# Optimization experiments

Hardware: AMD Instinct MI355X
Metric: run time of the kernel (lower is better)

Reference implementation:

```python
import jax, jax.numpy as jnp
import numpy as np

B, L1, L2, D = 128, 256, 256, 768
NEG = -10000.0
EPS = 1e-8


def setup_inputs() -> dict:
    key = jax.random.key(0)
    k1, k2, k3, k4 = jax.random.split(key, 4)
    v1 = jax.random.normal(k1, (B, L1, D), dtype=jnp.float32)
    v2 = jax.random.normal(k2, (B, L2, D), dtype=jnp.float32)
    # masks from random valid lengths in [L//2, L]
    len1 = jax.random.randint(k3, (B,), L1 // 2, L1 + 1)
    len2 = jax.random.randint(k4, (B,), L2 // 2, L2 + 1)
    mask1 = (jnp.arange(L1)[None, :] < len1[:, None]).astype(jnp.float32)
    mask2 = (jnp.arange(L2)[None, :] < len2[:, None]).astype(jnp.float32)
    return {"v1": v1, "mask1": mask1, "v2": v2, "mask2": mask2}


def reference(v1, mask1, v2, mask2):
    # alignment matrix [B, L1, L2]
    match = jnp.einsum('bld,bmd->blm', v1, v2)
    pair_mask = (mask1[:, :, None] * mask2[:, None, :]) > 0
    match = jnp.where(pair_mask, match, NEG)
    # attention over side 1: negative max-pool over L2, scaled
    s1 = -jnp.max(match, axis=2) / 100.0            # [B, L1]
    s1 = jnp.where(mask1 > 0, s1, NEG)
    attn1 = jax.nn.softmax(s1, axis=1)
    p1 = jnp.einsum('bld,bl->bd', v1, attn1)        # [B, D]
    # attention over side 2: negative max-pool over L1, scaled
    s2 = -jnp.max(match, axis=1) / 100.0            # [B, L2]
    s2 = jnp.where(mask2 > 0, s2, NEG)
    attn2 = jax.nn.softmax(s2, axis=1)
    p2 = jnp.einsum('bmd,bm->bd', v2, attn2)        # [B, D]
    # torch.nn.functional.cosine_similarity semantics (per-vector norm clamp)
    n1 = jnp.maximum(jnp.linalg.norm(p1, axis=-1), EPS)
    n2 = jnp.maximum(jnp.linalg.norm(p2, axis=-1), EPS)
    return jnp.sum(p1 * p2, axis=-1) / (n1 * n2)
```

## Files before the change

### kernel.cpp

```cpp
#include <hip/hip_runtime.h>


#define B_   128
#define L_   256
#define D_   768
#define NEGV (-10000.0f)

typedef _Float16 f16x8 __attribute__((ext_vector_type(8)));
typedef __fp16   h16x2 __attribute__((ext_vector_type(2)));
typedef float    f32x4 __attribute__((ext_vector_type(4)));

#define BT   128
#define BKF  64
#define NKT  (D_ / BKF)
#define LDH  72

__device__ __forceinline__ unsigned fmap(float f) {
    unsigned u = __float_as_uint(f);
    return (u & 0x80000000u) ? ~u : (u | 0x80000000u);
}
__device__ __forceinline__ float fdecode(unsigned u) {
    return __uint_as_float((u & 0x80000000u) ? (u ^ 0x80000000u) : ~u);
}
__device__ __forceinline__ float wred_max(float v) {
    #pragma unroll
    for (int o = 32; o; o >>= 1) v = fmaxf(v, __shfl_xor(v, o));
    return v;
}
__device__ __forceinline__ float wred_sum(float v) {
    #pragma unroll
    for (int o = 32; o; o >>= 1) v += __shfl_xor(v, o);
    return v;
}

__device__ __forceinline__ f16x8 cvt8(float4 a, float4 b) {
    union { h16x2 h2[4]; f16x8 h8; } u;
    u.h2[0] = __builtin_amdgcn_cvt_pkrtz(a.x, a.y);
    u.h2[1] = __builtin_amdgcn_cvt_pkrtz(a.z, a.w);
    u.h2[2] = __builtin_amdgcn_cvt_pkrtz(b.x, b.y);
    u.h2[3] = __builtin_amdgcn_cvt_pkrtz(b.z, b.w);
    return u.h8;
}

__global__ __launch_bounds__(512, 2)
void k_match_max(const float* __restrict__ v1, const float* __restrict__ m1,
                 const float* __restrict__ v2, const float* __restrict__ m2,
                 unsigned* __restrict__ ru1, unsigned* __restrict__ ru2)
{
    __shared__ __align__(16) _Float16 As[2][BT * LDH];
    __shared__ __align__(16) _Float16 Bs[2][BT * LDH];
    __shared__ unsigned rU[BT], cU[BT];
    __shared__ float m1s[BT], m2s[BT];

    const int bid = blockIdx.x;
    const int wg  = (bid & 7) * 64 + (bid >> 3);
    const int b = wg >> 2, ti = (wg >> 1) & 1, tj = wg & 1;

    const int t = threadIdx.x;
    const int lane = t & 63, w = t >> 6;
    const int wr = w >> 1, wc = w & 1;
    const int fr = lane & 15, fg = lane >> 4;

    if (t < BT) {
        rU[t] = 0u; cU[t] = 0u;
        m1s[t] = m1[b * L_ + ti * BT + t];
        m2s[t] = m2[b * L_ + tj * BT + t];
    }

    const int grow = t >> 2;
    const int c4   = t & 3;
    const float* ga = v1 + ((size_t)b * L_ + ti * BT + grow) * D_ + c4 * 16;
    const float* gb = v2 + ((size_t)b * L_ + tj * BT + grow) * D_ + c4 * 16;

    float4 ra[4], rb[4];

    #define GLOAD(kt) do {                                                    \
        const float* A_ = ga + (kt) * BKF;                                    \
        const float* C_ = gb + (kt) * BKF;                                    \
        ra[0] = *(const float4*)(A_);      ra[1] = *(const float4*)(A_ + 4);  \
        ra[2] = *(const float4*)(A_ + 8);  ra[3] = *(const float4*)(A_ + 12); \
        rb[0] = *(const float4*)(C_);      rb[1] = *(const float4*)(C_ + 4);  \
        rb[2] = *(const float4*)(C_ + 8);  rb[3] = *(const float4*)(C_ + 12); \
    } while (0)

    #define DSWRITE(buf) do {                                                 \
        _Float16* da = &As[buf][grow * LDH + c4 * 16];                        \
        _Float16* db = &Bs[buf][grow * LDH + c4 * 16];                        \
        *(f16x8*)da       = cvt8(ra[0], ra[1]);                               \
        *(f16x8*)(da + 8) = cvt8(ra[2], ra[3]);                               \
        *(f16x8*)db       = cvt8(rb[0], rb[1]);                               \
        *(f16x8*)(db + 8) = cvt8(rb[2], rb[3]);                               \
    } while (0)

    f32x4 acc[2][4] = {};
    GLOAD(0);
    DSWRITE(0);
    __syncthreads();
    int cur = 0;
    for (int kt = 0; kt < NKT; ++kt) {
        if (kt + 1 < NKT) GLOAD(kt + 1);
        __builtin_amdgcn_sched_barrier(0);
        #pragma unroll
        for (int ks = 0; ks < 2; ++ks) {
            f16x8 af[2], bf[4];
            #pragma unroll
            for (int i = 0; i < 2; ++i) {
                int r1 = wr * 32 + i * 16 + fr;
                af[i] = *(const f16x8*)&As[cur][r1 * LDH + ks * 32 + fg * 8];
            }
            #pragma unroll
            for (int j = 0; j < 4; ++j) {
                int r2 = wc * 64 + j * 16 + fr;
                bf[j] = *(const f16x8*)&Bs[cur][r2 * LDH + ks * 32 + fg * 8];
            }
            #pragma unroll
            for (int i = 0; i < 2; ++i)
                #pragma unroll
                for (int j = 0; j < 4; ++j)
                    acc[i][j] = __builtin_amdgcn_mfma_f32_16x16x32_f16(af[i], bf[j], acc[i][j], 0, 0, 0);
        }
        __builtin_amdgcn_sched_barrier(0);
        if (kt + 1 < NKT) DSWRITE(cur ^ 1);
        __syncthreads();
        cur ^= 1;
    }
    #undef GLOAD
    #undef DSWRITE

    #pragma unroll
    for (int i = 0; i < 2; ++i)
        #pragma unroll
        for (int r = 0; r < 4; ++r) {
            int row = wr * 32 + i * 16 + fg * 4 + r;
            bool rv = m1s[row] > 0.f;
            float mx = NEGV;
            #pragma unroll
            for (int j = 0; j < 4; ++j) {
                int col = wc * 64 + j * 16 + fr;
                float vv = (rv && m2s[col] > 0.f) ? acc[i][j][r] : NEGV;
                mx = fmaxf(mx, vv);
            }
            atomicMax(&rU[row], fmap(mx));
        }
    #pragma unroll
    for (int j = 0; j < 4; ++j) {
        int col = wc * 64 + j * 16 + fr;
        bool cv = m2s[col] > 0.f;
        float mx = NEGV;
        #pragma unroll
        for (int i = 0; i < 2; ++i)
            #pragma unroll
            for (int r = 0; r < 4; ++r) {
                int row = wr * 32 + i * 16 + fg * 4 + r;
                float vv = (cv && m1s[row] > 0.f) ? acc[i][j][r] : NEGV;
                mx = fmaxf(mx, vv);
            }
        atomicMax(&cU[col], fmap(mx));
    }
    __syncthreads();
    if (t < BT)            atomicMax(&ru1[b * L_ + ti * BT + t], rU[t]);
    else if (t < 2 * BT)   atomicMax(&ru2[b * L_ + tj * BT + (t - BT)], cU[t - BT]);
}

__global__ __launch_bounds__(256)
void k_attn_pool(const float* __restrict__ v1, const float* __restrict__ m1,
                 const float* __restrict__ v2, const float* __restrict__ m2,
                 const unsigned* __restrict__ ru1, const unsigned* __restrict__ ru2,
                 float* __restrict__ pout)
{
    const int lin = (int)blockIdx.x;
    const int swz = (lin & 7) * 96 + (lin >> 3);
    const int b = swz / 6, rem = swz % 6, side = rem / 3, chunk = rem % 3;

    const float* v     = side ? v2 : v1;
    const float* mk    = side ? m2 : m1;
    const unsigned* ru = side ? ru2 : ru1;
    const int t = threadIdx.x, lane = t & 63, w = t >> 6;

    __shared__ float attn[L_];
    __shared__ float sred[4];

    float mkv = mk[b * L_ + t];
    float s = (mkv > 0.f) ? (-fdecode(ru[b * L_ + t]) / 100.0f) : NEGV;

    float wm = wred_max(s);
    if (lane == 0) sred[w] = wm;
    __syncthreads();
    float mx = fmaxf(fmaxf(sred[0], sred[1]), fmaxf(sred[2], sred[3]));
    float e = expf(s - mx);
    __syncthreads();
    float ws = wred_sum(e);
    if (lane == 0) sred[w] = ws;
    __syncthreads();
    float sum = sred[0] + sred[1] + sred[2] + sred[3];
    attn[t] = e / sum;
    __syncthreads();

    const int d = chunk * 256 + t;
    const float* vb = v + (size_t)b * L_ * D_ + d;
    float p = 0.f;
    #pragma unroll 8
    for (int l = 0; l < L_; ++l) p += attn[l] * vb[(size_t)l * D_];
    pout[((size_t)b * 2 + side) * D_ + d] = p;
}

__global__ __launch_bounds__(256)
void k_cos(const float* __restrict__ pout, float* __restrict__ out)
{
    const int b = blockIdx.x, t = threadIdx.x, lane = t & 63, w = t >> 6;
    const float* p1 = pout + (size_t)b * 2 * D_;
    const float* p2 = p1 + D_;
    float dot = 0.f, n1 = 0.f, n2 = 0.f;
    for (int d = t; d < D_; d += 256) {
        float a = p1[d], c = p2[d];
        dot += a * c; n1 += a * a; n2 += c * c;
    }
    dot = wred_sum(dot); n1 = wred_sum(n1); n2 = wred_sum(n2);
    __shared__ float sd[4], sa[4], sc[4];
    if (lane == 0) { sd[w] = dot; sa[w] = n1; sc[w] = n2; }
    __syncthreads();
    if (t == 0) {
        float dd = sd[0] + sd[1] + sd[2] + sd[3];
        float aa = sa[0] + sa[1] + sa[2] + sa[3];
        float cc = sc[0] + sc[1] + sc[2] + sc[3];
        out[b] = dd / (fmaxf(sqrtf(aa), 1e-8f) * fmaxf(sqrtf(cc), 1e-8f));
    }
}

extern "C" void kernel_launch(void* const* d_in, const int* in_sizes, int n_in,
                              void* d_out, int out_size, void* d_ws, size_t ws_size,
                              hipStream_t stream)
{
    const float* v1 = (const float*)d_in[0];
    const float* m1 = (const float*)d_in[1];
    const float* v2 = (const float*)d_in[2];
    const float* m2 = (const float*)d_in[3];
    float* out = (float*)d_out;

    unsigned* ru1 = (unsigned*)d_ws;
    unsigned* ru2 = ru1 + (size_t)B_ * L_;
    float*    pout = (float*)(ru2 + (size_t)B_ * L_);

    (void)hipMemsetAsync(d_ws, 0, 2 * (size_t)B_ * L_ * sizeof(unsigned), stream);

    k_match_max<<<dim3((L_ / BT) * (L_ / BT) * B_), 512, 0, stream>>>(v1, m1, v2, m2, ru1, ru2);

    k_attn_pool<<<dim3(B_ * 2 * 3), 256, 0, stream>>>(v1, m1, v2, m2, ru1, ru2, pout);

    k_cos<<<B_, 256, 0, stream>>>(pout, out);
}
```

Before: 78.23 us.

## Fuse match-max, attention pooling and cosine into one kernel via last-block counter

Merges the three kernels into one. Each tile block writes its partial row and column maxima to per-tile slots instead of issuing global atomicMax. A per-batch atomic counter picks the last of the four tile blocks, which then computes both softmaxes, the pooled vectors and the cosine similarity in-block. This removes two kernel launches and shrinks the memset, but the tail work for each batch now runs on only 128 blocks, with each thread looping over three D-chunks serially. That could lengthen the critical path compared with the 768-block pooling kernel.

```diff
diff --git a/kernel.cpp b/kernel.cpp
--- a/kernel.cpp
+++ b/kernel.cpp
@@ -14,6 +14,7 @@
 #define BKF  64
 #define NKT  (D_ / BKF)
 #define LDH  72
+#define NBH  (BT * LDH)
 
 __device__ __forceinline__ unsigned fmap(float f) {
     unsigned u = __float_as_uint(f);
@@ -43,14 +44,19 @@
 }
 
 __global__ __launch_bounds__(512, 2)
-void k_match_max(const float* __restrict__ v1, const float* __restrict__ m1,
-                 const float* __restrict__ v2, const float* __restrict__ m2,
-                 unsigned* __restrict__ ru1, unsigned* __restrict__ ru2)
+void k_fused(const float* __restrict__ v1, const float* __restrict__ m1,
+             const float* __restrict__ v2, const float* __restrict__ m2,
+             float* __restrict__ rmax_p, float* __restrict__ cmax_p,
+             unsigned* __restrict__ cnt, float* __restrict__ out)
 {
-    __shared__ __align__(16) _Float16 As[2][BT * LDH];
-    __shared__ __align__(16) _Float16 Bs[2][BT * LDH];
+    __shared__ __align__(16) char smem[2 * 2 * NBH * 2];
     __shared__ unsigned rU[BT], cU[BT];
     __shared__ float m1s[BT], m2s[BT];
+    __shared__ float sred[8], sd[8], sa[8], sc2[8];
+    __shared__ int islast;
+
+    _Float16* AsB = (_Float16*)smem;
+    _Float16* BsB = (_Float16*)(smem + 2 * NBH * 2);
 
     const int bid = blockIdx.x;
     const int wg  = (bid & 7) * 64 + (bid >> 3);
@@ -84,8 +90,8 @@
     } while (0)
 
     #define DSWRITE(buf) do {                                                 \
-        _Float16* da = &As[buf][grow * LDH + c4 * 16];                        \
-        _Float16* db = &Bs[buf][grow * LDH + c4 * 16];                        \
+        _Float16* da = AsB + (buf) * NBH + grow * LDH + c4 * 16;              \
+        _Float16* db = BsB + (buf) * NBH + grow * LDH + c4 * 16;              \
         *(f16x8*)da       = cvt8(ra[0], ra[1]);                               \
         *(f16x8*)(da + 8) = cvt8(ra[2], ra[3]);                               \
         *(f16x8*)db       = cvt8(rb[0], rb[1]);                               \
@@ -106,12 +112,12 @@
             #pragma unroll
             for (int i = 0; i < 2; ++i) {
                 int r1 = wr * 32 + i * 16 + fr;
-                af[i] = *(const f16x8*)&As[cur][r1 * LDH + ks * 32 + fg * 8];
+                af[i] = *(const f16x8*)&AsB[cur * NBH + r1 * LDH + ks * 32 + fg * 8];
             }
             #pragma unroll
             for (int j = 0; j < 4; ++j) {
                 int r2 = wc * 64 + j * 16 + fr;
-                bf[j] = *(const f16x8*)&Bs[cur][r2 * LDH + ks * 32 + fg * 8];
+                bf[j] = *(const f16x8*)&BsB[cur * NBH + r2 * LDH + ks * 32 + fg * 8];
             }
             #pragma unroll
             for (int i = 0; i < 2; ++i)
@@ -158,71 +164,66 @@
         atomicMax(&cU[col], fmap(mx));
     }
     __syncthreads();
-    if (t < BT)            atomicMax(&ru1[b * L_ + ti * BT + t], rU[t]);
-    else if (t < 2 * BT)   atomicMax(&ru2[b * L_ + tj * BT + (t - BT)], cU[t - BT]);
-}
-
-__global__ __launch_bounds__(256)
-void k_attn_pool(const float* __restrict__ v1, const float* __restrict__ m1,
-                 const float* __restrict__ v2, const float* __restrict__ m2,
-                 const unsigned* __restrict__ ru1, const unsigned* __restrict__ ru2,
-                 float* __restrict__ pout)
-{
-    const int lin = (int)blockIdx.x;
-    const int swz = (lin & 7) * 96 + (lin >> 3);
-    const int b = swz / 6, rem = swz % 6, side = rem / 3, chunk = rem % 3;
-
-    const float* v     = side ? v2 : v1;
-    const float* mk    = side ? m2 : m1;
-    const unsigned* ru = side ? ru2 : ru1;
-    const int t = threadIdx.x, lane = t & 63, w = t >> 6;
-
-    __shared__ float attn[L_];
-    __shared__ float sred[4];
-
-    float mkv = mk[b * L_ + t];
-    float s = (mkv > 0.f) ? (-fdecode(ru[b * L_ + t]) / 100.0f) : NEGV;
+
+    if (t < BT)            rmax_p[((size_t)b * 2 + tj) * L_ + ti * BT + t]      = fdecode(rU[t]);
+    else if (t < 2 * BT)   cmax_p[((size_t)b * 2 + ti) * L_ + tj * BT + (t - BT)] = fdecode(cU[t - BT]);
+    __threadfence();
+    __syncthreads();
+    if (t == 0) islast = (atomicAdd(&cnt[b], 1u) == 3u);
+    __syncthreads();
+    if (!islast) return;
+    __threadfence();
+
+    float* attnb = (float*)smem;
+    float* pbuf  = (float*)(smem + 2048);
+    const int h = t >> 8;
+    const int l = t & 255;
+
+    volatile const float* rp = rmax_p + (size_t)b * 2 * L_;
+    volatile const float* cp = cmax_p + (size_t)b * 2 * L_;
+    float mkv = (h ? m2 : m1)[b * L_ + l];
+    float mxv = h ? fmaxf(cp[l], cp[L_ + l]) : fmaxf(rp[l], rp[L_ + l]);
+    float s = (mkv > 0.f) ? (-mxv * 0.01f) : NEGV;
 
     float wm = wred_max(s);
     if (lane == 0) sred[w] = wm;
     __syncthreads();
-    float mx = fmaxf(fmaxf(sred[0], sred[1]), fmaxf(sred[2], sred[3]));
+    float mx = fmaxf(fmaxf(sred[h * 4 + 0], sred[h * 4 + 1]),
+                     fmaxf(sred[h * 4 + 2], sred[h * 4 + 3]));
     float e = expf(s - mx);
     __syncthreads();
-    float ws = wred_sum(e);
-    if (lane == 0) sred[w] = ws;
-    __syncthreads();
-    float sum = sred[0] + sred[1] + sred[2] + sred[3];
-    attn[t] = e / sum;
-    __syncthreads();
-
-    const int d = chunk * 256 + t;
-    const float* vb = v + (size_t)b * L_ * D_ + d;
-    float p = 0.f;
-    #pragma unroll 8
-    for (int l = 0; l < L_; ++l) p += attn[l] * vb[(size_t)l * D_];
-    pout[((size_t)b * 2 + side) * D_ + d] = p;
-}
-
-__global__ __launch_bounds__(256)
-void k_cos(const float* __restrict__ pout, float* __restrict__ out)
-{
-    const int b = blockIdx.x, t = threadIdx.x, lane = t & 63, w = t >> 6;
-    const float* p1 = pout + (size_t)b * 2 * D_;
-    const float* p2 = p1 + D_;
+    float wsum = wred_sum(e);
+    if (lane == 0) sred[w] = wsum;
+    __syncthreads();
+    float sum = sred[h * 4 + 0] + sred[h * 4 + 1] + sred[h * 4 + 2] + sred[h * 4 + 3];
+    attnb[h * 256 + l] = e / sum;
+    __syncthreads();
+
+    const float* vsrc = (h ? v2 : v1) + (size_t)b * L_ * D_;
+    const float* an = attnb + h * 256;
+    #pragma unroll
+    for (int chunk = 0; chunk < 3; ++chunk) {
+        int d = chunk * 256 + l;
+        const float* vb = vsrc + d;
+        float p = 0.f;
+        #pragma unroll 8
+        for (int ll = 0; ll < L_; ++ll) p += an[ll] * vb[(size_t)ll * D_];
+        pbuf[h * 768 + d] = p;
+    }
+    __syncthreads();
+
     float dot = 0.f, n1 = 0.f, n2 = 0.f;
-    for (int d = t; d < D_; d += 256) {
-        float a = p1[d], c = p2[d];
+    for (int d = t; d < D_; d += 512) {
+        float a = pbuf[d], c = pbuf[768 + d];
         dot += a * c; n1 += a * a; n2 += c * c;
     }
     dot = wred_sum(dot); n1 = wred_sum(n1); n2 = wred_sum(n2);
-    __shared__ float sd[4], sa[4], sc[4];
-    if (lane == 0) { sd[w] = dot; sa[w] = n1; sc[w] = n2; }
+    if (lane == 0) { sd[w] = dot; sa[w] = n1; sc2[w] = n2; }
     __syncthreads();
     if (t == 0) {
-        float dd = sd[0] + sd[1] + sd[2] + sd[3];
-        float aa = sa[0] + sa[1] + sa[2] + sa[3];
-        float cc = sc[0] + sc[1] + sc[2] + sc[3];
+        float dd = 0.f, aa = 0.f, cc = 0.f;
+        #pragma unroll
+        for (int i = 0; i < 8; ++i) { dd += sd[i]; aa += sa[i]; cc += sc2[i]; }
         out[b] = dd / (fmaxf(sqrtf(aa), 1e-8f) * fmaxf(sqrtf(cc), 1e-8f));
     }
 }
@@ -237,15 +238,11 @@
     const float* m2 = (const float*)d_in[3];
     float* out = (float*)d_out;
 
-    unsigned* ru1 = (unsigned*)d_ws;
-    unsigned* ru2 = ru1 + (size_t)B_ * L_;
-    float*    pout = (float*)(ru2 + (size_t)B_ * L_);
-
-    (void)hipMemsetAsync(d_ws, 0, 2 * (size_t)B_ * L_ * sizeof(unsigned), stream);
-
-    k_match_max<<<dim3((L_ / BT) * (L_ / BT) * B_), 512, 0, stream>>>(v1, m1, v2, m2, ru1, ru2);
-
-    k_attn_pool<<<dim3(B_ * 2 * 3), 256, 0, stream>>>(v1, m1, v2, m2, ru1, ru2, pout);
-
-    k_cos<<<B_, 256, 0, stream>>>(pout, out);
-}
+    unsigned* cnt    = (unsigned*)d_ws;
+    float*    rmax_p = (float*)((char*)d_ws + 512);
+    float*    cmax_p = rmax_p + (size_t)B_ * 2 * L_;
+
+    (void)hipMemsetAsync(d_ws, 0, 512, stream);
+
+    k_fused<<<dim3(4 * B_), 512, 0, stream>>>(v1, m1, v2, m2, rmax_p, cmax_p, cnt, out);
+}
```

After: 177.0 us. 126% more time.

## Use 128x256 match tiles, write partial maxima directly and drop memset

Applied to the files above, without the earlier changes.

The match kernel now has each 1024-thread block compute a 128-row by full-256-column tile per batch, replacing the 128x128 tiles with 512 threads. Row maxima are complete within a block and are written directly. Column maxima go out as two partials that the pooling kernel combines, which removes the global atomics and the workspace memset. In exchange it launches only 256 large blocks, roughly one per CU, which can lower occupancy and latency hiding. The larger B tile also raises LDS use.

```diff
diff --git a/kernel.cpp b/kernel.cpp
--- a/kernel.cpp
+++ b/kernel.cpp
@@ -10,7 +10,7 @@
 typedef __fp16   h16x2 __attribute__((ext_vector_type(2)));
 typedef float    f32x4 __attribute__((ext_vector_type(4)));
 
-#define BT   128
+#define BTR  128
 #define BKF  64
 #define NKT  (D_ / BKF)
 #define LDH  72
@@ -32,7 +32,6 @@
     for (int o = 32; o; o >>= 1) v += __shfl_xor(v, o);
     return v;
 }
-
 __device__ __forceinline__ f16x8 cvt8(float4 a, float4 b) {
     union { h16x2 h2[4]; f16x8 h8; } u;
     u.h2[0] = __builtin_amdgcn_cvt_pkrtz(a.x, a.y);
@@ -42,52 +41,46 @@
     return u.h8;
 }
 
-__global__ __launch_bounds__(512, 2)
-void k_match_max(const float* __restrict__ v1, const float* __restrict__ m1,
-                 const float* __restrict__ v2, const float* __restrict__ m2,
-                 unsigned* __restrict__ ru1, unsigned* __restrict__ ru2)
-{
-    __shared__ __align__(16) _Float16 As[2][BT * LDH];
-    __shared__ __align__(16) _Float16 Bs[2][BT * LDH];
-    __shared__ unsigned rU[BT], cU[BT];
-    __shared__ float m1s[BT], m2s[BT];
+__global__ __launch_bounds__(1024, 1)
+void k_match(const float* __restrict__ v1, const float* __restrict__ m1,
+             const float* __restrict__ v2, const float* __restrict__ m2,
+             float* __restrict__ rmax, float* __restrict__ cmax_p)
+{
+    __shared__ __align__(16) _Float16 As[2][BTR * LDH];
+    __shared__ __align__(16) _Float16 Bs[2][L_ * LDH];
+    __shared__ unsigned rU[BTR], cU[L_];
+    __shared__ float m1s[BTR], m2s[L_];
 
     const int bid = blockIdx.x;
-    const int wg  = (bid & 7) * 64 + (bid >> 3);
-    const int b = wg >> 2, ti = (wg >> 1) & 1, tj = wg & 1;
+    const int wg  = (bid & 7) * 32 + (bid >> 3);
+    const int b = wg >> 1, rh = wg & 1;
 
     const int t = threadIdx.x;
     const int lane = t & 63, w = t >> 6;
-    const int wr = w >> 1, wc = w & 1;
+    const int wr = w >> 2, wc = w & 3;
     const int fr = lane & 15, fg = lane >> 4;
 
-    if (t < BT) {
-        rU[t] = 0u; cU[t] = 0u;
-        m1s[t] = m1[b * L_ + ti * BT + t];
-        m2s[t] = m2[b * L_ + tj * BT + t];
-    }
-
-    const int grow = t >> 2;
-    const int c4   = t & 3;
-    const float* ga = v1 + ((size_t)b * L_ + ti * BT + grow) * D_ + c4 * 16;
-    const float* gb = v2 + ((size_t)b * L_ + tj * BT + grow) * D_ + c4 * 16;
-
-    float4 ra[4], rb[4];
+    if (t < BTR) { rU[t] = 0u; m1s[t] = m1[b * L_ + rh * BTR + t]; }
+    if (t < L_)  { cU[t] = 0u; m2s[t] = m2[b * L_ + t]; }
+
+    const int a_r = t >> 3, a_c = (t & 7) * 8;
+    const int b_r = t >> 2, b_c = (t & 3) * 16;
+    const float* ga = v1 + ((size_t)b * L_ + rh * BTR + a_r) * D_ + a_c;
+    const float* gb = v2 + ((size_t)b * L_ + b_r) * D_ + b_c;
+
+    float4 ra[2], rb[4];
 
     #define GLOAD(kt) do {                                                    \
         const float* A_ = ga + (kt) * BKF;                                    \
         const float* C_ = gb + (kt) * BKF;                                    \
         ra[0] = *(const float4*)(A_);      ra[1] = *(const float4*)(A_ + 4);  \
-        ra[2] = *(const float4*)(A_ + 8);  ra[3] = *(const float4*)(A_ + 12); \
         rb[0] = *(const float4*)(C_);      rb[1] = *(const float4*)(C_ + 4);  \
         rb[2] = *(const float4*)(C_ + 8);  rb[3] = *(const float4*)(C_ + 12); \
     } while (0)
 
     #define DSWRITE(buf) do {                                                 \
-        _Float16* da = &As[buf][grow * LDH + c4 * 16];                        \
-        _Float16* db = &Bs[buf][grow * LDH + c4 * 16];                        \
-        *(f16x8*)da       = cvt8(ra[0], ra[1]);                               \
-        *(f16x8*)(da + 8) = cvt8(ra[2], ra[3]);                               \
+        *(f16x8*)&As[buf][a_r * LDH + a_c] = cvt8(ra[0], ra[1]);              \
+        _Float16* db = &Bs[buf][b_r * LDH + b_c];                             \
         *(f16x8*)db       = cvt8(rb[0], rb[1]);                               \
         *(f16x8*)(db + 8) = cvt8(rb[2], rb[3]);                               \
     } while (0)
@@ -158,30 +151,33 @@
         atomicMax(&cU[col], fmap(mx));
     }
     __syncthreads();
-    if (t < BT)            atomicMax(&ru1[b * L_ + ti * BT + t], rU[t]);
-    else if (t < 2 * BT)   atomicMax(&ru2[b * L_ + tj * BT + (t - BT)], cU[t - BT]);
+
+    if (t < BTR)                rmax[b * L_ + rh * BTR + t] = fdecode(rU[t]);
+    else if (t < BTR + L_)      cmax_p[((size_t)b * 2 + rh) * L_ + (t - BTR)] = fdecode(cU[t - BTR]);
 }
 
 __global__ __launch_bounds__(256)
 void k_attn_pool(const float* __restrict__ v1, const float* __restrict__ m1,
                  const float* __restrict__ v2, const float* __restrict__ m2,
-                 const unsigned* __restrict__ ru1, const unsigned* __restrict__ ru2,
+                 const float* __restrict__ rmax, const float* __restrict__ cmax_p,
                  float* __restrict__ pout)
 {
     const int lin = (int)blockIdx.x;
     const int swz = (lin & 7) * 96 + (lin >> 3);
     const int b = swz / 6, rem = swz % 6, side = rem / 3, chunk = rem % 3;
 
-    const float* v     = side ? v2 : v1;
-    const float* mk    = side ? m2 : m1;
-    const unsigned* ru = side ? ru2 : ru1;
+    const float* v  = side ? v2 : v1;
+    const float* mk = side ? m2 : m1;
     const int t = threadIdx.x, lane = t & 63, w = t >> 6;
 
     __shared__ float attn[L_];
     __shared__ float sred[4];
 
     float mkv = mk[b * L_ + t];
-    float s = (mkv > 0.f) ? (-fdecode(ru[b * L_ + t]) / 100.0f) : NEGV;
+    float mxv = side ? fmaxf(cmax_p[((size_t)b * 2) * L_ + t],
+                             cmax_p[((size_t)b * 2 + 1) * L_ + t])
+                     : rmax[b * L_ + t];
+    float s = (mkv > 0.f) ? (-mxv * 0.01f) : NEGV;
 
     float wm = wred_max(s);
     if (lane == 0) sred[w] = wm;
@@ -237,15 +233,13 @@
     const float* m2 = (const float*)d_in[3];
     float* out = (float*)d_out;
 
-    unsigned* ru1 = (unsigned*)d_ws;
-    unsigned* ru2 = ru1 + (size_t)B_ * L_;
-    float*    pout = (float*)(ru2 + (size_t)B_ * L_);
-
-    (void)hipMemsetAsync(d_ws, 0, 2 * (size_t)B_ * L_ * sizeof(unsigned), stream);
-
-    k_match_max<<<dim3((L_ / BT) * (L_ / BT) * B_), 512, 0, stream>>>(v1, m1, v2, m2, ru1, ru2);
-
-    k_attn_pool<<<dim3(B_ * 2 * 3), 256, 0, stream>>>(v1, m1, v2, m2, ru1, ru2, pout);
+    float* rmax   = (float*)d_ws;
+    float* cmax_p = rmax + (size_t)B_ * L_;
+    float* pout   = cmax_p + (size_t)B_ * 2 * L_;
+
+    k_match<<<dim3(2 * B_), 1024, 0, stream>>>(v1, m1, v2, m2, rmax, cmax_p);
+
+    k_attn_pool<<<dim3(B_ * 2 * 3), 256, 0, stream>>>(v1, m1, v2, m2, rmax, cmax_p, pout);
 
     k_cos<<<B_, 256, 0, stream>>>(pout, out);
 }
```

After: 73.99 us. -5.4%, faster.
